# Kernel tuning notes

Measured on AMD Instinct MI355X. Metric: run time of the kernel, lower is better.

## Reference

```python
import jax, jax.numpy as jnp
import numpy as np

B, I, O, H = 1024, 128, 128, 5  # batch, input_size, output_size, hidden_size


def setup_inputs() -> dict:
    key = jax.random.key(0)
    ks = jax.random.split(key, 7)
    s = 0.3  # modest init scale, like torch default Linear init range
    return {
        "x": jax.random.normal(ks[0], (B, I), dtype=jnp.float32),
        # stacked per-edge MLP params: one tiny MLP per (output_node, input_node) edge
        "W1": jax.random.normal(ks[1], (O, I, H), dtype=jnp.float32) * s,  # Linear(1,H).weight
        "B1": jax.random.normal(ks[2], (O, I, H), dtype=jnp.float32) * s,
        "W2": jax.random.normal(ks[3], (O, I, H, H), dtype=jnp.float32) * s,  # Linear(H,H).weight (out,in)
        "B2": jax.random.normal(ks[4], (O, I, H), dtype=jnp.float32) * s,
        "W3": jax.random.normal(ks[5], (O, I, H), dtype=jnp.float32) * s,  # Linear(H,1).weight
        "B3": jax.random.normal(ks[6], (O, I), dtype=jnp.float32) * s,
    }


def reference(x, W1, B1, W2, B2, W3, B3):
    # Per-edge MLP, vectorized over all O*I edges at once.
    lrelu = lambda t: jax.nn.leaky_relu(t, negative_slope=0.01)  # torch LeakyReLU default
    # layer 1: scalar input -> H. [B,O,I,H]
    h1 = lrelu(x[:, None, :, None] * W1 + B1)
    # layer 2: H -> H per edge. torch Linear: y = h @ W.T, W is (out,in) -> contract 'in' axis
    h2 = lrelu(jnp.einsum("boih,oikh->boik", h1, W2) + B2)
    # layer 3: H -> scalar per edge, then sum over input nodes j
    y_edge = jnp.einsum("boih,oih->boi", h2, W3) + B3  # [B,O,I]
    return y_edge.sum(axis=2)  # [B,O]
```

## Files before the change

kernel.cpp:

```cpp
#include <hip/hip_runtime.h>

#define Bsz 1024
#define Isz 128
#define Osz 128
#define Hsz 5
#define PSTRIDE 48
#define GB 64
#define NG (Bsz / GB)

__global__ __launch_bounds__(256)
void repack_kernel(const float* __restrict__ W1, const float* __restrict__ B1,
                   const float* __restrict__ W2, const float* __restrict__ B2,
                   const float* __restrict__ W3, const float* __restrict__ B3,
                   float* __restrict__ P) {
    int idx = blockIdx.x * 256 + threadIdx.x;
    if (idx >= Osz * Isz * PSTRIDE) return;
    int e = idx / PSTRIDE;
    int s = idx - e * PSTRIDE;
    float v = 0.0f;
    if (s < 5)        v = W1[e * 5 + s];
    else if (s < 10)  v = B1[e * 5 + (s - 5)];
    else if (s < 35)  v = W2[e * 25 + (s - 10)];
    else if (s < 40)  v = B2[e * 5 + (s - 35)];
    else if (s < 45)  v = W3[e * 5 + (s - 40)];
    else if (s == 45) v = B3[e];
    P[idx] = v;
}

__global__ __launch_bounds__(256, 4)
void kan_kernel(const float* __restrict__ x, const float* __restrict__ P,
                float* __restrict__ out) {
    __shared__ float xs[GB * Isz];
    __shared__ float partial[4 * 64];

    const int tid = threadIdx.x;
    const int ob  = blockIdx.x & 63;
    const int g   = blockIdx.x >> 6;
    const int b0  = g * GB;
    const int w   = tid >> 6;
    const int l   = tid & 63;
    const int o   = 2 * ob + (w >> 1);
    const int i   = 64 * (w & 1) + l;

    {
        const float4* xg = (const float4*)(x + (size_t)b0 * Isz);
        float4* xs4 = (float4*)xs;
        #pragma unroll
        for (int j = 0; j < (GB * Isz / 4) / 256; ++j)
            xs4[tid + 256 * j] = xg[tid + 256 * j];
    }

    float p[PSTRIDE];
    {
        const float4* pr = (const float4*)(P + (size_t)(o * Isz + i) * PSTRIDE);
        #pragma unroll
        for (int j = 0; j < PSTRIDE / 4; ++j)
            ((float4*)p)[j] = pr[j];
    }
    __syncthreads();

    float res = 0.0f;

    for (int bl = 0; bl < GB; bl += 4) {
        float a[4], y[4];
        #pragma unroll
        for (int u = 0; u < 4; ++u) a[u] = xs[(bl + u) * Isz + i];

        #pragma unroll
        for (int u = 0; u < 4; ++u) {
            float h1[Hsz];
            #pragma unroll
            for (int h = 0; h < Hsz; ++h) {
                float v = fmaf(a[u], p[h], p[5 + h]);
                h1[h] = fmaxf(v, 0.01f * v);
            }
            float yy = p[45];
            #pragma unroll
            for (int k = 0; k < Hsz; ++k) {
                float s = p[35 + k];
                #pragma unroll
                for (int h = 0; h < Hsz; ++h)
                    s = fmaf(h1[h], p[10 + k * Hsz + h], s);
                s = fmaxf(s, 0.01f * s);
                yy = fmaf(s, p[40 + k], yy);
            }
            y[u] = yy;
        }

        #pragma unroll
        for (int u = 0; u < 4; ++u) {
            float s = y[u];
            #pragma unroll
            for (int m = 1; m <= 32; m <<= 1)
                s += __shfl_xor(s, m, 64);
            if (l == bl + u) res = s;
        }
    }

    partial[w * 64 + l] = res;
    __syncthreads();

    if (tid < 128) {
        const int bl = tid & 63;
        const int oo = tid >> 6;
        const float v = partial[(2 * oo) * 64 + bl] + partial[(2 * oo + 1) * 64 + bl];
        out[(size_t)(b0 + bl) * Osz + (2 * ob + oo)] = v;
    }
}

extern "C" void kernel_launch(void* const* d_in, const int* in_sizes, int n_in,
                              void* d_out, int out_size, void* d_ws, size_t ws_size,
                              hipStream_t stream) {
    const float* x  = (const float*)d_in[0];
    const float* W1 = (const float*)d_in[1];
    const float* B1 = (const float*)d_in[2];
    const float* W2 = (const float*)d_in[3];
    const float* B2 = (const float*)d_in[4];
    const float* W3 = (const float*)d_in[5];
    const float* B3 = (const float*)d_in[6];
    float* out = (float*)d_out;
    float* P   = (float*)d_ws;

    const int n = Osz * Isz * PSTRIDE;
    repack_kernel<<<dim3((n + 255) / 256), dim3(256), 0, stream>>>(W1, B1, W2, B2, W3, B3, P);

    const dim3 grid((Osz / 2) * NG);
    kan_kernel<<<grid, dim3(256), 0, stream>>>(x, P, out);
}
```

Measured before the change: 96.95 us.

## Drop parameter repack kernel, read weights directly, use DPP wave reductions

Removes the separate repack kernel and its workspace round trip; each thread now loads its edge's weights straight from the original arrays with strided scalar loads. Replaces the shuffle-based butterfly reduction with DPP row operations plus row_bcast and a readlane from lane 63. Raises the batch unroll from 4 to 8. This saves a kernel launch and a global write/read pass, but the weight loads are uncoalesced scalar loads instead of float4, and the larger unroll adds register pressure.

```diff
diff --git a/kernel.cpp b/kernel.cpp
--- a/kernel.cpp
+++ b/kernel.cpp
@@ -4,31 +4,31 @@
 #define Isz 128
 #define Osz 128
 #define Hsz 5
-#define PSTRIDE 48
 #define GB 64
 #define NG (Bsz / GB)
+#define UF 8
 
-__global__ __launch_bounds__(256)
-void repack_kernel(const float* __restrict__ W1, const float* __restrict__ B1,
-                   const float* __restrict__ W2, const float* __restrict__ B2,
-                   const float* __restrict__ W3, const float* __restrict__ B3,
-                   float* __restrict__ P) {
-    int idx = blockIdx.x * 256 + threadIdx.x;
-    if (idx >= Osz * Isz * PSTRIDE) return;
-    int e = idx / PSTRIDE;
-    int s = idx - e * PSTRIDE;
-    float v = 0.0f;
-    if (s < 5)        v = W1[e * 5 + s];
-    else if (s < 10)  v = B1[e * 5 + (s - 5)];
-    else if (s < 35)  v = W2[e * 25 + (s - 10)];
-    else if (s < 40)  v = B2[e * 5 + (s - 35)];
-    else if (s < 45)  v = W3[e * 5 + (s - 40)];
-    else if (s == 45) v = B3[e];
-    P[idx] = v;
+template <int CTRL>
+__device__ __forceinline__ float dpp_add(float s) {
+    int t = __builtin_amdgcn_update_dpp(0, __builtin_bit_cast(int, s),
+                                        CTRL, 0xf, 0xf, true);
+    return s + __builtin_bit_cast(float, t);
+}
+__device__ __forceinline__ float wave_sum64_lane63(float s) {
+    s = dpp_add<0xB1>(s);
+    s = dpp_add<0x4E>(s);
+    s = dpp_add<0x141>(s);
+    s = dpp_add<0x140>(s);
+    s = dpp_add<0x142>(s);
+    s = dpp_add<0x143>(s);
+    return s;
 }
 
 __global__ __launch_bounds__(256, 4)
-void kan_kernel(const float* __restrict__ x, const float* __restrict__ P,
+void kan_kernel(const float* __restrict__ x,
+                const float* __restrict__ W1, const float* __restrict__ B1,
+                const float* __restrict__ W2, const float* __restrict__ B2,
+                const float* __restrict__ W3, const float* __restrict__ B3,
                 float* __restrict__ out) {
     __shared__ float xs[GB * Isz];
     __shared__ float partial[4 * 64];
@@ -41,6 +41,7 @@
     const int l   = tid & 63;
     const int o   = 2 * ob + (w >> 1);
     const int i   = 64 * (w & 1) + l;
+    const int e   = o * Isz + i;
 
     {
         const float4* xg = (const float4*)(x + (size_t)b0 * Isz);
@@ -50,50 +51,53 @@
             xs4[tid + 256 * j] = xg[tid + 256 * j];
     }
 
-    float p[PSTRIDE];
-    {
-        const float4* pr = (const float4*)(P + (size_t)(o * Isz + i) * PSTRIDE);
-        #pragma unroll
-        for (int j = 0; j < PSTRIDE / 4; ++j)
-            ((float4*)p)[j] = pr[j];
+    float w1[Hsz], b1[Hsz], w2[Hsz * Hsz], b2[Hsz], w3[Hsz];
+    #pragma unroll
+    for (int h = 0; h < Hsz; ++h) {
+        w1[h] = W1[(size_t)e * Hsz + h];
+        b1[h] = B1[(size_t)e * Hsz + h];
+        b2[h] = B2[(size_t)e * Hsz + h];
+        w3[h] = W3[(size_t)e * Hsz + h];
     }
+    #pragma unroll
+    for (int j = 0; j < Hsz * Hsz; ++j) w2[j] = W2[(size_t)e * Hsz * Hsz + j];
+    const float b3v = B3[e];
+
     __syncthreads();
 
     float res = 0.0f;
 
-    for (int bl = 0; bl < GB; bl += 4) {
-        float a[4], y[4];
+    for (int bl = 0; bl < GB; bl += UF) {
+        float y[UF];
         #pragma unroll
-        for (int u = 0; u < 4; ++u) a[u] = xs[(bl + u) * Isz + i];
+        for (int u = 0; u < UF; ++u) {
+            const float a = xs[(bl + u) * Isz + i];
 
-        #pragma unroll
-        for (int u = 0; u < 4; ++u) {
             float h1[Hsz];
             #pragma unroll
             for (int h = 0; h < Hsz; ++h) {
-                float v = fmaf(a[u], p[h], p[5 + h]);
+                float v = fmaf(a, w1[h], b1[h]);
                 h1[h] = fmaxf(v, 0.01f * v);
             }
-            float yy = p[45];
+            float yy = b3v;
             #pragma unroll
             for (int k = 0; k < Hsz; ++k) {
-                float s = p[35 + k];
+                float s = b2[k];
                 #pragma unroll
                 for (int h = 0; h < Hsz; ++h)
-                    s = fmaf(h1[h], p[10 + k * Hsz + h], s);
+                    s = fmaf(h1[h], w2[k * Hsz + h], s);
                 s = fmaxf(s, 0.01f * s);
-                yy = fmaf(s, p[40 + k], yy);
+                yy = fmaf(s, w3[k], yy);
             }
             y[u] = yy;
         }
 
         #pragma unroll
-        for (int u = 0; u < 4; ++u) {
-            float s = y[u];
-            #pragma unroll
-            for (int m = 1; m <= 32; m <<= 1)
-                s += __shfl_xor(s, m, 64);
-            if (l == bl + u) res = s;
+        for (int u = 0; u < UF; ++u) {
+            const float s = wave_sum64_lane63(y[u]);
+            const float tot = __builtin_bit_cast(float,
+                __builtin_amdgcn_readlane(__builtin_bit_cast(int, s), 63));
+            if (l == bl + u) res = tot;
         }
     }
 
@@ -119,11 +123,7 @@
     const float* W3 = (const float*)d_in[5];
     const float* B3 = (const float*)d_in[6];
     float* out = (float*)d_out;
-    float* P   = (float*)d_ws;
-
-    const int n = Osz * Isz * PSTRIDE;
-    repack_kernel<<<dim3((n + 255) / 256), dim3(256), 0, stream>>>(W1, B1, W2, B2, W3, B3, P);
 
     const dim3 grid((Osz / 2) * NG);
-    kan_kernel<<<grid, dim3(256), 0, stream>>>(x, P, out);
+    kan_kernel<<<grid, dim3(256), 0, stream>>>(x, W1, B1, W2, B2, W3, B3, out);
 }
```

Measured after the change: 92.01 us. 5.1% less time.
